# Kernel tuning notes

Hardware: AMD Instinct MI355X
Metric: run time of the kernel (lower is better)

Reference implementation:

```python
import jax, jax.numpy as jnp
import numpy as np

EPS = 1e-5


def _resize_bilinear_ac(x, h, w):
    # bilinear, align_corners=True; x: [B, C, H, W]
    H, W = x.shape[2], x.shape[3]
    ys = jnp.linspace(0.0, H - 1.0, h)
    xs = jnp.linspace(0.0, W - 1.0, w)
    y0 = jnp.floor(ys).astype(jnp.int32)
    x0 = jnp.floor(xs).astype(jnp.int32)
    y1 = jnp.clip(y0 + 1, 0, H - 1)
    x1 = jnp.clip(x0 + 1, 0, W - 1)
    wy = (ys - y0.astype(ys.dtype))[None, None, :, None]
    wx = (xs - x0.astype(xs.dtype))[None, None, None, :]
    rows0 = x[:, :, y0, :]  # [B,C,h,W]
    rows1 = x[:, :, y1, :]
    a = rows0[:, :, :, x0]
    b = rows0[:, :, :, x1]
    c = rows1[:, :, :, x0]
    d = rows1[:, :, :, x1]
    top = a * (1.0 - wx) + b * wx
    bot = c * (1.0 - wx) + d * wx
    return top * (1.0 - wy) + bot * wy


def _conv3x3(x, w):
    return jax.lax.conv_general_dilated(
        x, w, window_strides=(1, 1), padding=[(1, 1), (1, 1)],
        dimension_numbers=('NCHW', 'OIHW', 'NCHW'))


def _bn(x, g, b, m, v):
    scale = (g / jnp.sqrt(v + EPS))[None, :, None, None]
    shift = (b - m * g / jnp.sqrt(v + EPS))[None, :, None, None]
    return x * scale + shift


def setup_inputs() -> dict:
    key = jax.random.key(0)
    ks = jax.random.split(key, 12)
    B = 8
    xt = jax.random.normal(ks[0], (B, 512, 32, 32), jnp.float32)
    xm = jax.random.normal(ks[1], (B, 512, 64, 64), jnp.float32)
    xl = jax.random.normal(ks[2], (B, 256, 128, 128), jnp.float32)
    alpha = jnp.ones((1,), jnp.float32)
    w0 = jax.random.normal(ks[3], (512, 512, 3, 3), jnp.float32) * 0.02
    g0 = jnp.abs(jax.random.normal(ks[4], (512,), jnp.float32)) * 0.1 + 1.0
    b0 = jax.random.normal(ks[5], (512,), jnp.float32) * 0.1
    m0 = jax.random.normal(ks[6], (512,), jnp.float32) * 0.1
    v0 = jnp.abs(jax.random.normal(ks[7], (512,), jnp.float32)) * 0.1 + 1.0
    w1 = jax.random.normal(ks[8], (256, 512, 3, 3), jnp.float32) * 0.02
    g1 = jnp.abs(jax.random.normal(ks[9], (256,), jnp.float32)) * 0.1 + 1.0
    b1 = jax.random.normal(ks[10], (256,), jnp.float32) * 0.1
    m1 = jax.random.normal(ks[11], (256,), jnp.float32) * 0.1
    v1 = jnp.abs(jax.random.normal(jax.random.fold_in(key, 99), (256,), jnp.float32)) * 0.1 + 1.0
    return {"xt": xt, "xm": xm, "xl": xl, "alpha": alpha,
            "w0": w0, "g0": g0, "b0": b0, "m0": m0, "v0": v0,
            "w1": w1, "g1": g1, "b1": b1, "m1": m1, "v1": v1}


def reference(xt, xm, xl, alpha, w0, g0, b0, m0, v0, w1, g1, b1, m1, v1):
    # DecoderModule.forward: upsample xt to xm size (align_corners=True),
    # fuse with alpha-weighted skip, conv0(512->512,BN,ReLU), conv1(512->256,BN,ReLU).
    # xl is accepted but unused in this forward (as in the source).
    h, w = xm.shape[2], xm.shape[3]
    xup = _resize_bilinear_ac(xt, h, w)
    xfuse = xup + alpha[0] * xm
    x = jax.nn.relu(_bn(_conv3x3(xfuse, w0), g0, b0, m0, v0))
    xt_fea = jax.nn.relu(_bn(_conv3x3(x, w1), g1, b1, m1, v1))
    return xt_fea
```

## Files before the change

### kernel.cpp

```cpp
#include <hip/hip_runtime.h>
#include <stdint.h>

#define EPSV 1e-5f

#define CPLANE 278784

using floatx4 = __attribute__((ext_vector_type(4))) float;
using short8  = __attribute__((ext_vector_type(8))) short;

#define GLD(gp, lp) __builtin_amdgcn_global_load_lds( \
    (const __attribute__((address_space(1))) void*)(gp), \
    (__attribute__((address_space(3))) void*)(lp), 16, 0, 0)

__device__ __forceinline__ unsigned short f2bf(float f) {
  union { float f; unsigned int u; } x; x.f = f;
  unsigned int r = x.u + 0x7fffu + ((x.u >> 16) & 1u);
  return (unsigned short)(r >> 16);
}

__global__ __launch_bounds__(256) void border_zero_kernel(
    unsigned short* __restrict__ Xp0, unsigned short* __restrict__ Xp1) {
  int idx = blockIdx.x * 256 + threadIdx.x;
  int k = idx % 260;
  int rest = idx / 260;
  int cc = rest & 63;
  int b = rest >> 6;
  int py, px;
  if (k < 66)       { py = 0;  px = k; }
  else if (k < 132) { py = 65; px = k - 66; }
  else { int k2 = k - 132; py = 1 + (k2 >> 1); px = (k2 & 1) ? 65 : 0; }
  int off = cc * CPLANE + ((b * 66 + py) * 66 + px) * 8;
  short8 z = {};
  *(short8*)(Xp0 + off) = z;
  *(short8*)(Xp1 + off) = z;
}

__global__ __launch_bounds__(256) void fuse_upsample_kernel(
    const float* __restrict__ xt, const float* __restrict__ xm,
    const float* __restrict__ alpha, unsigned short* __restrict__ Xp) {
  __shared__ float sm[32 * 66];
  __shared__ float st[2 * 32 * 34];

  const int tid = threadIdx.x;
  const int ct = blockIdx.x & 15;
  const int y  = (blockIdx.x >> 4) & 63;
  const int b  = blockIdx.x >> 10;
  const int c0 = ct * 32;

  const float fy = y * (31.0f / 63.0f);
  const int y0 = (int)fy;
  const float wy = fy - (float)y0;
  const int y1 = min(y0 + 1, 31);

  {
    const int cb = (tid >> 6) * 8;
    const int xi = tid & 63;
#pragma unroll
    for (int j = 0; j < 8; ++j) {
      int c = cb + j;
      sm[c * 66 + xi] = xm[(((b << 9) + c0 + c) << 12) + (y << 6) + xi];
    }
  }
#pragma unroll
  for (int j = 0; j < 8; ++j) {
    int idx = j * 256 + tid;
    int xi = idx & 31, cc = (idx >> 5) & 31, h = idx >> 10;
    int yr = h ? y1 : y0;
    st[h * 1088 + cc * 34 + xi] =
        xt[(((b << 9) + c0 + cc) << 10) + (yr << 5) + xi];
  }
  __syncthreads();

  const float a = alpha[0];
  const int xo = tid & 63;
  const int cl = tid >> 6;
  const float fx = xo * (31.0f / 63.0f);
  const int x0 = (int)fx;
  const float wx = fx - (float)x0;
  const int x1 = min(x0 + 1, 31);
  short8 ov;
#pragma unroll
  for (int j = 0; j < 8; ++j) {
    int c = cl * 8 + j;
    float t0 = st[c * 34 + x0], t1 = st[c * 34 + x1];
    float u0 = st[1088 + c * 34 + x0], u1 = st[1088 + c * 34 + x1];
    float top = t0 * (1.0f - wx) + t1 * wx;
    float bot = u0 * (1.0f - wx) + u1 * wx;
    float up = top * (1.0f - wy) + bot * wy;
    float val = up + a * sm[c * 66 + xo];
    ov[j] = (short)f2bf(val);
  }
  *(short8*)(Xp + ((c0 >> 3) + cl) * CPLANE +
             ((b * 66 + y + 1) * 66 + xo + 1) * 8) = ov;
}

template <int COUT>
__global__ __launch_bounds__(256) void prep_w_kernel(
    const float* __restrict__ w, unsigned short* __restrict__ Wg) {
  __shared__ unsigned short l[4608];
  const int o = blockIdx.x, t = threadIdx.x;
  const float* src = w + o * 4608;
#pragma unroll
  for (int j = 0; j < 18; ++j) {
    int idx = j * 256 + t;
    l[(idx % 9) * 512 + idx / 9] = f2bf(src[idx]);
  }
  __syncthreads();
#pragma unroll
  for (int tap = 0; tap < 9; ++tap) {
    int cc = t >> 2;
    int off = ((tap * 64 + cc) * COUT + o) * 8 + ((2 * t) & 7);
    *(unsigned int*)(Wg + off) = *(const unsigned int*)(l + (tap << 9) + 2 * t);
  }
}

template <int COUT, int CTILE, bool FINAL>
__global__ __launch_bounds__(256) void conv3x3_kernel(
    const unsigned short* __restrict__ Xp, const unsigned short* __restrict__ Wg,
    const float* __restrict__ gamma, const float* __restrict__ beta,
    const float* __restrict__ mean, const float* __restrict__ var,
    unsigned short* __restrict__ OutPad, float* __restrict__ OutF) {
  constexpr int NCT = COUT / CTILE;
  constexpr int NI  = CTILE / 32;
  __shared__ unsigned short Abuf[16896];
  __shared__ unsigned short Bbuf0[CTILE * 64];
  __shared__ unsigned short Bbuf1[CTILE * 64];

  const int tid = threadIdx.x;
  const int ptile = (int)blockIdx.x / NCT;
  const int ctile = (int)blockIdx.x % NCT;
  const int p0 = ptile * 128;
  const int w = tid >> 6;
  const int lane = tid & 63;

  const int pb = p0 >> 12;
  const int yb = (p0 >> 6) & 63;
  const int arowg = ((pb * 66 + yb) * 66) * 8;

  const int fi = lane & 15;
  const int kc = lane >> 4;
  const int wm = w >> 1, wn = w & 1;
  const int aLane = kc * 2112 + (wm + 1) * 528 + (fi + 1) * 8;
  const int bLane = kc * CTILE * 8 + (wn * (CTILE / 2) + fi) * 8;

  floatx4 acc[4][NI] = {};

  auto stageA = [&](int cg) {
#pragma unroll
    for (int kk = 0; kk < 2; ++kk) {
      const int kc2 = 2 * w + kk;
      const unsigned short* g = Xp + (cg * 8 + kc2) * CPLANE + arowg + lane * 8;
      unsigned short* d = Abuf + kc2 * 2112;
#pragma unroll
      for (int rr = 0; rr < 4; ++rr) {
        GLD(g + rr * 528,      d + rr * 528);
        GLD(g + rr * 528 + 16, d + rr * 528 + 16);
      }
    }
  };
  auto stageB = [&](int tap, int cg, unsigned short* dst) {
#pragma unroll
    for (int kk = 0; kk < 2; ++kk) {
      const int kc2 = 2 * w + kk;
      const unsigned short* g =
          Wg + ((tap * 64 + cg * 8 + kc2) * COUT + ctile * CTILE + lane) * 8;
#pragma unroll
      for (int half = 0; half < CTILE / 64; ++half)
        GLD(g + half * 64 * 8, dst + (kc2 * CTILE + half * 64) * 8);
    }
  };
  auto compute = [&](const unsigned short* Bsel, int dy, int dx) {
#pragma unroll
    for (int t = 0; t < 2; ++t) {
      short8 af[4];
#pragma unroll
      for (int mi = 0; mi < 4; ++mi)
        af[mi] = *(const short8*)(Abuf + aLane + t * 8448 + dy * 528 +
                                  (mi * 16 + dx) * 8);
      short8 bfr[NI];
#pragma unroll
      for (int ni = 0; ni < NI; ++ni)
        bfr[ni] = *(const short8*)(Bsel + bLane + t * CTILE * 32 + ni * 128);
#pragma unroll
      for (int mi = 0; mi < 4; ++mi)
#pragma unroll
        for (int ni = 0; ni < NI; ++ni)
          acc[mi][ni] = __builtin_amdgcn_mfma_f32_16x16x32_bf16(
              af[mi], bfr[ni], acc[mi][ni], 0, 0, 0);
    }
  };

  int buf = 0;
  stageA(0);
  stageB(0, 0, Bbuf0);
  __syncthreads();
  for (int cg = 0; cg < 8; ++cg) {
#pragma unroll
    for (int tap = 0; tap < 9; ++tap) {
      unsigned short* cur = buf ? Bbuf1 : Bbuf0;
      unsigned short* nxt = buf ? Bbuf0 : Bbuf1;
      if (tap < 8)      stageB(tap + 1, cg, nxt);
      else if (cg < 7)  stageB(0, cg + 1, nxt);
      compute(cur, tap / 3 - 1, tap % 3 - 1);
      __syncthreads();
      buf ^= 1;
    }
    if (cg < 7) {
      stageA(cg + 1);
      __syncthreads();
    }
  }

#pragma unroll
  for (int ni = 0; ni < NI; ++ni) {
    const int co = ctile * CTILE + wn * (CTILE / 2) + ni * 16 + fi;
    const float sc = gamma[co] / sqrtf(var[co] + EPSV);
    const float sh2 = beta[co] - mean[co] * sc;
#pragma unroll
    for (int mi = 0; mi < 4; ++mi) {
      const int p = p0 + wm * 64 + mi * 16 + kc * 4;
      const int pbb = p >> 12;
      const int prem = p & 4095;
      if constexpr (FINAL) {
        floatx4 o;
#pragma unroll
        for (int r = 0; r < 4; ++r) o[r] = fmaxf(acc[mi][ni][r] * sc + sh2, 0.0f);
        *(floatx4*)(OutF + ((pbb * COUT + co) << 12) + prem) = o;
      } else {
        const int py = prem >> 6, px = prem & 63;
        unsigned short* dst = OutPad + (co >> 3) * CPLANE +
            ((pbb * 66 + py + 1) * 66 + px + 1) * 8 + (co & 7);
#pragma unroll
        for (int r = 0; r < 4; ++r)
          dst[r * 8] = f2bf(fmaxf(acc[mi][ni][r] * sc + sh2, 0.0f));
      }
    }
  }
}

extern "C" void kernel_launch(void* const* d_in, const int* in_sizes, int n_in,
                              void* d_out, int out_size, void* d_ws, size_t ws_size,
                              hipStream_t stream) {
  const float* xt    = (const float*)d_in[0];
  const float* xm    = (const float*)d_in[1];
  const float* alpha = (const float*)d_in[3];
  const float* w0    = (const float*)d_in[4];
  const float* g0    = (const float*)d_in[5];
  const float* b0    = (const float*)d_in[6];
  const float* m0    = (const float*)d_in[7];
  const float* v0    = (const float*)d_in[8];
  const float* w1    = (const float*)d_in[9];
  const float* g1    = (const float*)d_in[10];
  const float* b1    = (const float*)d_in[11];
  const float* m1    = (const float*)d_in[12];
  const float* v1    = (const float*)d_in[13];
  float* out = (float*)d_out;

  char* ws = (char*)d_ws;
  unsigned short* Xp0 = (unsigned short*)(ws);
  unsigned short* Xp1 = (unsigned short*)(ws + 35684352);
  unsigned short* Wg0 = (unsigned short*)(ws + 2 * 35684352);
  unsigned short* Wg1 = (unsigned short*)(ws + 2 * 35684352 + 4718592);

  border_zero_kernel<<<520, 256, 0, stream>>>(Xp0, Xp1);
  prep_w_kernel<512><<<512, 256, 0, stream>>>(w0, Wg0);
  prep_w_kernel<256><<<256, 256, 0, stream>>>(w1, Wg1);
  fuse_upsample_kernel<<<8192, 256, 0, stream>>>(xt, xm, alpha, Xp0);
  conv3x3_kernel<512, 128, false><<<1024, 256, 0, stream>>>(Xp0, Wg0, g0, b0, m0, v0, Xp1, nullptr);
  conv3x3_kernel<256, 64, true><<<1024, 256, 0, stream>>>(Xp1, Wg1, g1, b1, m1, v1, nullptr, out);
}
```

Measured before the change: 484.5 us.

## Load conv weights directly to registers and double-buffer the activation tile in LDS

Weight fragments are now prefetched from global memory straight into registers, one tap ahead, instead of being staged through double-buffered LDS. The activation tile gets two LDS buffers with a padded stride, so the next channel group loads while the current one is computed. This removes the per-tap barrier, leaving one per channel group, and sets launch bounds to two blocks per CU. The cost is higher register pressure from the register-held B fragments and more redundant global weight reads across waves, which may cause spills or limit occupancy.

```diff
diff --git a/kernel.cpp b/kernel.cpp
--- a/kernel.cpp
+++ b/kernel.cpp
@@ -115,16 +115,16 @@
 }
 
 template <int COUT, int CTILE, bool FINAL>
-__global__ __launch_bounds__(256) void conv3x3_kernel(
+__global__ __launch_bounds__(256, 2) void conv3x3_kernel(
     const unsigned short* __restrict__ Xp, const unsigned short* __restrict__ Wg,
     const float* __restrict__ gamma, const float* __restrict__ beta,
     const float* __restrict__ mean, const float* __restrict__ var,
     unsigned short* __restrict__ OutPad, float* __restrict__ OutF) {
   constexpr int NCT = COUT / CTILE;
   constexpr int NI  = CTILE / 32;
-  __shared__ unsigned short Abuf[16896];
-  __shared__ unsigned short Bbuf0[CTILE * 64];
-  __shared__ unsigned short Bbuf1[CTILE * 64];
+  constexpr int KCS = 2128;
+  constexpr int ABUF = 8 * KCS;
+  __shared__ __align__(64) unsigned short Abuf[2][ABUF];
 
   const int tid = threadIdx.x;
   const int ptile = (int)blockIdx.x / NCT;
@@ -140,17 +140,17 @@
   const int fi = lane & 15;
   const int kc = lane >> 4;
   const int wm = w >> 1, wn = w & 1;
-  const int aLane = kc * 2112 + (wm + 1) * 528 + (fi + 1) * 8;
-  const int bLane = kc * CTILE * 8 + (wn * (CTILE / 2) + fi) * 8;
+  const int aLane = kc * KCS + (wm + 1) * 528 + (fi + 1) * 8;
 
   floatx4 acc[4][NI] = {};
-
-  auto stageA = [&](int cg) {
+  short8 bcur[2][NI], bnxt[2][NI];
+
+  auto stageA = [&](int cg, int bsel) {
 #pragma unroll
     for (int kk = 0; kk < 2; ++kk) {
       const int kc2 = 2 * w + kk;
       const unsigned short* g = Xp + (cg * 8 + kc2) * CPLANE + arowg + lane * 8;
-      unsigned short* d = Abuf + kc2 * 2112;
+      unsigned short* d = &Abuf[bsel][0] + kc2 * KCS;
 #pragma unroll
       for (int rr = 0; rr < 4; ++rr) {
         GLD(g + rr * 528,      d + rr * 528);
@@ -158,57 +158,54 @@
       }
     }
   };
-  auto stageB = [&](int tap, int cg, unsigned short* dst) {
-#pragma unroll
-    for (int kk = 0; kk < 2; ++kk) {
-      const int kc2 = 2 * w + kk;
-      const unsigned short* g =
-          Wg + ((tap * 64 + cg * 8 + kc2) * COUT + ctile * CTILE + lane) * 8;
-#pragma unroll
-      for (int half = 0; half < CTILE / 64; ++half)
-        GLD(g + half * 64 * 8, dst + (kc2 * CTILE + half * 64) * 8);
-    }
+
+  auto loadB = [&](int tap, int cg, short8 (&dst)[2][NI]) {
+    const unsigned short* base =
+        Wg + ((tap * 64 + cg * 8 + kc) * COUT +
+              ctile * CTILE + wn * (CTILE / 2) + fi) * 8;
+#pragma unroll
+    for (int t = 0; t < 2; ++t)
+#pragma unroll
+      for (int ni = 0; ni < NI; ++ni)
+        dst[t][ni] = *(const short8*)(base + (t * 4 * COUT + ni * 16) * 8);
   };
-  auto compute = [&](const unsigned short* Bsel, int dy, int dx) {
+
+  auto compute = [&](int bsel, int dy, int dx) {
+    const unsigned short* ab = &Abuf[bsel][0] + aLane + dy * 528 + dx * 8;
 #pragma unroll
     for (int t = 0; t < 2; ++t) {
       short8 af[4];
 #pragma unroll
       for (int mi = 0; mi < 4; ++mi)
-        af[mi] = *(const short8*)(Abuf + aLane + t * 8448 + dy * 528 +
-                                  (mi * 16 + dx) * 8);
-      short8 bfr[NI];
-#pragma unroll
-      for (int ni = 0; ni < NI; ++ni)
-        bfr[ni] = *(const short8*)(Bsel + bLane + t * CTILE * 32 + ni * 128);
+        af[mi] = *(const short8*)(ab + t * (4 * KCS) + mi * 128);
 #pragma unroll
       for (int mi = 0; mi < 4; ++mi)
 #pragma unroll
         for (int ni = 0; ni < NI; ++ni)
           acc[mi][ni] = __builtin_amdgcn_mfma_f32_16x16x32_bf16(
-              af[mi], bfr[ni], acc[mi][ni], 0, 0, 0);
+              af[mi], bcur[t][ni], acc[mi][ni], 0, 0, 0);
     }
   };
 
-  int buf = 0;
-  stageA(0);
-  stageB(0, 0, Bbuf0);
+  stageA(0, 0);
+  loadB(0, 0, bcur);
   __syncthreads();
+
+  int cur = 0;
   for (int cg = 0; cg < 8; ++cg) {
+    if (cg < 7) stageA(cg + 1, cur ^ 1);
 #pragma unroll
     for (int tap = 0; tap < 9; ++tap) {
-      unsigned short* cur = buf ? Bbuf1 : Bbuf0;
-      unsigned short* nxt = buf ? Bbuf0 : Bbuf1;
-      if (tap < 8)      stageB(tap + 1, cg, nxt);
-      else if (cg < 7)  stageB(0, cg + 1, nxt);
+      if (tap < 8)      loadB(tap + 1, cg, bnxt);
+      else if (cg < 7)  loadB(0, cg + 1, bnxt);
       compute(cur, tap / 3 - 1, tap % 3 - 1);
-      __syncthreads();
-      buf ^= 1;
-    }
-    if (cg < 7) {
-      stageA(cg + 1);
-      __syncthreads();
-    }
+#pragma unroll
+      for (int t = 0; t < 2; ++t)
+#pragma unroll
+        for (int ni = 0; ni < NI; ++ni) bcur[t][ni] = bnxt[t][ni];
+    }
+    __syncthreads();
+    cur ^= 1;
   }
 
 #pragma unroll
```

New measurement: 544.4 us. +12.4%, slower.
